# Performance work log

Measured on AMD Instinct MI355X. Metric: run time of the kernel, lower is better.

The kernel has to match this reference:

```python
import jax, jax.numpy as jnp
import numpy as np

LN_EPS = 1e-5


def _ln(x, g, b):
    m = x.mean(-1, keepdims=True)
    v = ((x - m) ** 2).mean(-1, keepdims=True)
    return (x - m) * jax.lax.rsqrt(v + LN_EPS) * g + b


def _shift(x):
    # token shift: previous timestep, zeros at t=0. x: [B,T,C]
    return jnp.pad(x[:, :-1], ((0, 0), (1, 0), (0, 0)))


def _wkv(time_decay, time_first, k, v):
    # numerically-stable RWKV-v4 WKV scan. k, v: [B,T,C]
    B, T, C = k.shape
    decay = -jnp.exp(time_decay)  # [C], negative per-channel log-decay
    kT = jnp.transpose(k, (1, 0, 2))
    vT = jnp.transpose(v, (1, 0, 2))

    def step(carry, kv):
        aa, bb, pp = carry
        kt, vt = kv
        ww = time_first + kt
        p = jnp.maximum(pp, ww)
        e1 = jnp.exp(pp - p)
        e2 = jnp.exp(ww - p)
        out = (e1 * aa + e2 * vt) / (e1 * bb + e2)
        ww2 = pp + decay
        p2 = jnp.maximum(ww2, kt)
        f1 = jnp.exp(ww2 - p2)
        f2 = jnp.exp(kt - p2)
        return (f1 * aa + f2 * vt, f1 * bb + f2, p2), out

    init = (jnp.zeros((B, C), k.dtype), jnp.zeros((B, C), k.dtype),
            jnp.full((B, C), -1e38, k.dtype))
    _, out = jax.lax.scan(step, init, (kT, vT))
    return jnp.transpose(out, (1, 0, 2))


def setup_inputs() -> dict:
    key = jax.random.key(0)
    ks = jax.random.split(key, 24)
    B, T, Dv, Di = 32, 512, 512, 256
    F = Dv + Di
    H = 4 * F
    n = jax.random.normal
    u = jax.random.uniform(ks[4], (B, T, F, 2), minval=1e-6, maxval=1.0 - 1e-6)
    gumbel = -jnp.log(-jnp.log(u))
    sF = 1.0 / np.sqrt(F).astype(np.float32)
    sH = 1.0 / np.sqrt(H).astype(np.float32)
    return {
        'fv': n(ks[0], (B, T, Dv)),
        'fi': n(ks[1], (B, T, Di)),
        'fuse_W': n(ks[2], (F, 2 * F)) * sF,
        'fuse_b': jnp.zeros((2 * F,)),
        'gumbel': gumbel,
        'ln1_g': jnp.ones((F,)), 'ln1_b': jnp.zeros((F,)),
        'mix_k': jax.random.uniform(ks[5], (F,)),
        'mix_v': jax.random.uniform(ks[6], (F,)),
        'mix_r': jax.random.uniform(ks[7], (F,)),
        'time_decay': n(ks[8], (F,)) * 0.1 - 1.0,
        'time_first': n(ks[9], (F,)) * 0.1,
        'Wk': n(ks[10], (F, F)) * sF,
        'Wv': n(ks[11], (F, F)) * sF,
        'Wr': n(ks[12], (F, F)) * sF,
        'Wo': n(ks[13], (F, F)) * sF,
        'ln2_g': jnp.ones((F,)), 'ln2_b': jnp.zeros((F,)),
        'cmix_k': jax.random.uniform(ks[14], (F,)),
        'cmix_r': jax.random.uniform(ks[15], (F,)),
        'cWk': n(ks[16], (F, H)) * sF,
        'cWv': n(ks[17], (H, F)) * sH,
        'cWr': n(ks[18], (F, F)) * sF,
        'reg_W1': n(ks[19], (F, 128)) * sF,
        'reg_b1': jnp.zeros((128,)),
        'reg_W2': n(ks[20], (128, 6)) / np.sqrt(128).astype(np.float32),
        'reg_b2': jnp.zeros((6,)),
    }


def reference(fv, fi, fuse_W, fuse_b, gumbel, ln1_g, ln1_b, mix_k, mix_v, mix_r,
              time_decay, time_first, Wk, Wv, Wr, Wo, ln2_g, ln2_b,
              cmix_k, cmix_r, cWk, cWv, cWr, reg_W1, reg_b1, reg_W2, reg_b2):
    B, T, _ = fv.shape
    # ---- Fusion_module ('hard'): linear -> gumbel-softmax(hard, tau=1) gating
    feat = jnp.concatenate([fv, fi], axis=-1)            # [B,T,F]
    F = feat.shape[-1]
    logits = (feat @ fuse_W + fuse_b).reshape(B, T, F, 2)
    y = jax.nn.softmax(logits + gumbel, axis=-1)          # tau = 1
    hard = jax.nn.one_hot(jnp.argmax(y, -1), 2, dtype=y.dtype)
    mask = hard + y - jax.lax.stop_gradient(y)            # straight-through
    x = feat * mask[..., 0]

    # ---- RWKV block: time-mixing (WKV scan)
    xn = _ln(x, ln1_g, ln1_b)
    xs = _shift(xn)
    xk = xn * mix_k + xs * (1.0 - mix_k)
    xv = xn * mix_v + xs * (1.0 - mix_v)
    xr = xn * mix_r + xs * (1.0 - mix_r)
    k = xk @ Wk
    v = xv @ Wv
    r = jax.nn.sigmoid(xr @ Wr)
    x = x + (r * _wkv(time_decay, time_first, k, v)) @ Wo

    # ---- RWKV block: channel-mixing
    xn = _ln(x, ln2_g, ln2_b)
    xs = _shift(xn)
    xk = xn * cmix_k + xs * (1.0 - cmix_k)
    xr = xn * cmix_r + xs * (1.0 - cmix_r)
    kk = jnp.square(jax.nn.relu(xk @ cWk))
    x = x + jax.nn.sigmoid(xr @ cWr) * (kk @ cWv)

    h = x @ reg_W1 + reg_b1
    h = jnp.where(h > 0, h, 0.1 * h)
    return h @ reg_W2 + reg_b2                            # [B,T,6]
```

## Files before the change

kernel.cpp:

```cpp
#include <hip/hip_runtime.h>
#include <hip/hip_bf16.h>

#define BT 16384
#define FDIM 768
#define HDIM 3072

typedef __attribute__((ext_vector_type(8))) short bf16x8;
typedef __attribute__((ext_vector_type(4))) float f32x4;
typedef __attribute__((ext_vector_type(4))) int i32x4;
typedef __attribute__((ext_vector_type(2))) float f32x2;

__device__ inline float b2f(unsigned short u) {
  union { unsigned int i; float f; } x; x.i = ((unsigned int)u) << 16; return x.f;
}

#define GLOAD16(gptr, lptr)                                                    \
  __builtin_amdgcn_global_load_lds(                                            \
      (const __attribute__((address_space(1))) void*)(gptr),                   \
      (__attribute__((address_space(3))) void*)(lptr), 16, 0, 0)

__global__ void wconv5_kernel(const float* s0, const float* s1, const float* s2,
                              const float* s3, const float* s4,
                              __hip_bfloat16* d0, __hip_bfloat16* d1, __hip_bfloat16* d2,
                              __hip_bfloat16* d3, __hip_bfloat16* d4) {
  const float* in; __hip_bfloat16* out;
  switch (blockIdx.z) {
    case 0: in = s0; out = d0; break;
    case 1: in = s1; out = d1; break;
    case 2: in = s2; out = d2; break;
    case 3: in = s3; out = d3; break;
    default: in = s4; out = d4; break;
  }
  __shared__ float tile[32][33];
  int kb = blockIdx.x * 32, nb = blockIdx.y * 32;
  int tx = threadIdx.x & 31, ty = threadIdx.x >> 5;
#pragma unroll
  for (int i = 0; i < 4; ++i) {
    int k = ty + i * 8;
    tile[k][tx] = in[(size_t)(kb + k) * 768 + nb + tx];
  }
  __syncthreads();
#pragma unroll
  for (int i = 0; i < 4; ++i) {
    int n = ty + i * 8;
    out[(size_t)(nb + n) * 768 + kb + tx] = __float2bfloat16(tile[tx][n]);
  }
}

__global__ void wconv_kernel(const float* __restrict__ in, __hip_bfloat16* __restrict__ out,
                             int K, int N) {
  __shared__ float tile[32][33];
  int kb = blockIdx.x * 32, nb = blockIdx.y * 32;
  int tx = threadIdx.x & 31, ty = threadIdx.x >> 5;
#pragma unroll
  for (int i = 0; i < 4; ++i) {
    int k = ty + i * 8;
    tile[k][tx] = in[(size_t)(kb + k) * N + nb + tx];
  }
  __syncthreads();
#pragma unroll
  for (int i = 0; i < 4; ++i) {
    int n = ty + i * 8;
    out[(size_t)(nb + n) * K + kb + tx] = __float2bfloat16(tile[tx][n]);
  }
}

__global__ void wdsplit_kernel(const float* __restrict__ W, __hip_bfloat16* __restrict__ out) {
  __shared__ float tile[32][33];
  int kb = blockIdx.x * 32, nb = blockIdx.y * 32;
  int tx = threadIdx.x & 31, ty = threadIdx.x >> 5;
#pragma unroll
  for (int i = 0; i < 4; ++i) {
    int k = ty + i * 8;
    f32x2 p = ((const f32x2*)(W + (size_t)(kb + k) * 1536))[nb + tx];
    tile[k][tx] = p.x - p.y;
  }
  __syncthreads();
#pragma unroll
  for (int i = 0; i < 4; ++i) {
    int n = ty + i * 8;
    float d = tile[tx][n];
    __hip_bfloat16 h1 = __float2bfloat16(d);
    float r1 = d - __bfloat162float(h1);
    __hip_bfloat16 h2 = __float2bfloat16(r1);
    float r2 = r1 - __bfloat162float(h2);
    __hip_bfloat16 h3 = __float2bfloat16(r2);
    size_t base = (size_t)(nb + n) * 2304 + kb + tx;
    out[base] = h1; out[base + 768] = h2; out[base + 1536] = h3;
  }
}

__global__ void featsplit_kernel(const float* __restrict__ fv, const float* __restrict__ fi,
                                 __hip_bfloat16* __restrict__ FS) {
  int idx4 = blockIdx.x * 256 + threadIdx.x;
  int m = idx4 / 192, q = idx4 - m * 192;
  int c0 = q * 4;
  f32x4 f;
  if (c0 < 512) f = *(const f32x4*)(fv + (size_t)m * 512 + c0);
  else          f = *(const f32x4*)(fi + (size_t)m * 256 + (c0 - 512));
  unsigned short h1[4], h2[4], h3[4];
#pragma unroll
  for (int j = 0; j < 4; ++j) {
    float x = f[j];
    __hip_bfloat16 a = __float2bfloat16(x);
    float r1 = x - __bfloat162float(a);
    __hip_bfloat16 b = __float2bfloat16(r1);
    float r2 = r1 - __bfloat162float(b);
    __hip_bfloat16 c = __float2bfloat16(r2);
    h1[j] = *(unsigned short*)&a; h2[j] = *(unsigned short*)&b; h3[j] = *(unsigned short*)&c;
  }
  size_t base = (size_t)m * 2304 + c0;
  *(ushort4*)((unsigned short*)FS + base)        = make_ushort4(h1[0], h1[1], h1[2], h1[3]);
  *(ushort4*)((unsigned short*)FS + base + 768)  = make_ushort4(h2[0], h2[1], h2[2], h2[3]);
  *(ushort4*)((unsigned short*)FS + base + 1536) = make_ushort4(h3[0], h3[1], h3[2], h3[3]);
}

__global__ void lnmix3_kernel(const float* __restrict__ X, const float* __restrict__ g,
                              const float* __restrict__ b, const float* __restrict__ mk,
                              const float* __restrict__ mv, const float* __restrict__ mr,
                              __hip_bfloat16* __restrict__ AK, __hip_bfloat16* __restrict__ AV,
                              __hip_bfloat16* __restrict__ AR) {
  __shared__ float xn[5][768];
  int tok0 = blockIdx.x * 4;
  int w = threadIdx.x >> 6, lane = threadIdx.x & 63;
  int t = tok0 + w - 1;
  if (t >= 0) {
    const float* row = X + (size_t)t * 768;
    float vv[12]; float s = 0.f, s2 = 0.f;
#pragma unroll
    for (int i = 0; i < 12; ++i) { float x = row[lane + i * 64]; vv[i] = x; s += x; s2 += x * x; }
#pragma unroll
    for (int o = 32; o; o >>= 1) { s += __shfl_xor(s, o); s2 += __shfl_xor(s2, o); }
    float m = s * (1.0f / 768.0f);
    float var = s2 * (1.0f / 768.0f) - m * m;
    float inv = 1.0f / sqrtf(var + 1e-5f);
#pragma unroll
    for (int i = 0; i < 12; ++i) { int c = lane + i * 64; xn[w][c] = (vv[i] - m) * inv * g[c] + b[c]; }
  }
  __syncthreads();
  if (w >= 1) {
    int tt = tok0 + (w - 1);
    bool first = (tt & 511) == 0;
    size_t base = (size_t)tt * 768;
#pragma unroll
    for (int i = 0; i < 12; ++i) {
      int c = lane + i * 64;
      float a = xn[w][c];
      float sft = first ? 0.0f : xn[w - 1][c];
      float k = mk[c], v = mv[c], r = mr[c];
      AK[base + c] = __float2bfloat16(a * k + sft * (1.0f - k));
      AV[base + c] = __float2bfloat16(a * v + sft * (1.0f - v));
      AR[base + c] = __float2bfloat16(a * r + sft * (1.0f - r));
    }
  }
}

__global__ void lnmix2_kernel(const float* __restrict__ X, const float* __restrict__ g,
                              const float* __restrict__ b, const float* __restrict__ mk,
                              const float* __restrict__ mr,
                              __hip_bfloat16* __restrict__ AK, __hip_bfloat16* __restrict__ AR) {
  __shared__ float xn[5][768];
  int tok0 = blockIdx.x * 4;
  int w = threadIdx.x >> 6, lane = threadIdx.x & 63;
  int t = tok0 + w - 1;
  if (t >= 0) {
    const float* row = X + (size_t)t * 768;
    float vv[12]; float s = 0.f, s2 = 0.f;
#pragma unroll
    for (int i = 0; i < 12; ++i) { float x = row[lane + i * 64]; vv[i] = x; s += x; s2 += x * x; }
#pragma unroll
    for (int o = 32; o; o >>= 1) { s += __shfl_xor(s, o); s2 += __shfl_xor(s2, o); }
    float m = s * (1.0f / 768.0f);
    float var = s2 * (1.0f / 768.0f) - m * m;
    float inv = 1.0f / sqrtf(var + 1e-5f);
#pragma unroll
    for (int i = 0; i < 12; ++i) { int c = lane + i * 64; xn[w][c] = (vv[i] - m) * inv * g[c] + b[c]; }
  }
  __syncthreads();
  if (w >= 1) {
    int tt = tok0 + (w - 1);
    bool first = (tt & 511) == 0;
    size_t base = (size_t)tt * 768;
#pragma unroll
    for (int i = 0; i < 12; ++i) {
      int c = lane + i * 64;
      float a = xn[w][c];
      float sft = first ? 0.0f : xn[w - 1][c];
      float k = mk[c], r = mr[c];
      AK[base + c] = __float2bfloat16(a * k + sft * (1.0f - k));
      AR[base + c] = __float2bfloat16(a * r + sft * (1.0f - r));
    }
  }
}

__global__ void wkv_kernel(const float* __restrict__ K, const float* __restrict__ V,
                           const float* __restrict__ RP, const float* __restrict__ td,
                           const float* __restrict__ tfirst, __hip_bfloat16* __restrict__ RA) {
  int idx = blockIdx.x * 256 + threadIdx.x;
  int b = idx / 768, c = idx - b * 768;
  float decay = -__expf(td[c]);
  float u = tfirst[c];
  float aa = 0.f, bb = 0.f, pp = -1e38f;
  size_t o = (size_t)b * 512 * 768 + c;
  float ck[4], cv[4], cr[4], nk[4], nv[4], nr[4];
#pragma unroll
  for (int j = 0; j < 4; ++j) { size_t oj = o + (size_t)j * 768; ck[j] = K[oj]; cv[j] = V[oj]; cr[j] = RP[oj]; }
  size_t ob = o;
  for (int g = 0; g < 128; ++g) {
    size_t onext = (g == 127) ? o : ob + 3072;
#pragma unroll
    for (int j = 0; j < 4; ++j) {
      size_t oj = onext + (size_t)j * 768;
      nk[j] = K[oj]; nv[j] = V[oj]; nr[j] = RP[oj];
    }
#pragma unroll
    for (int j = 0; j < 4; ++j) {
      float kt = ck[j], vt = cv[j];
      float ww = u + kt;
      float p = fmaxf(pp, ww);
      float e1 = __expf(pp - p), e2 = __expf(ww - p);
      float wkv = (e1 * aa + e2 * vt) / (e1 * bb + e2);
      float ww2 = pp + decay;
      float p2 = fmaxf(ww2, kt);
      float f1 = __expf(ww2 - p2), f2 = __expf(kt - p2);
      aa = f1 * aa + f2 * vt; bb = f1 * bb + f2; pp = p2;
      float r = 1.0f / (1.0f + __expf(-cr[j]));
      RA[ob + (size_t)j * 768] = __float2bfloat16(r * wkv);
    }
#pragma unroll
    for (int j = 0; j < 4; ++j) { ck[j] = nk[j]; cv[j] = nv[j]; cr[j] = nr[j]; }
    ob += 3072;
  }
}

__global__ void reg2_kernel(const __hip_bfloat16* __restrict__ Hb, const float* __restrict__ W2,
                            const float* __restrict__ b2, float* __restrict__ out) {
  __shared__ float w[768];
  for (int i = threadIdx.x; i < 768; i += 256) w[i] = W2[i];
  __syncthreads();
  int m = blockIdx.x * 256 + threadIdx.x;
  float acc[6];
#pragma unroll
  for (int j = 0; j < 6; ++j) acc[j] = b2[j];
  const bf16x8* hr8 = (const bf16x8*)(Hb + (size_t)m * 128);
#pragma unroll
  for (int h8 = 0; h8 < 16; ++h8) {
    bf16x8 pk = hr8[h8];
#pragma unroll
    for (int e = 0; e < 8; ++e) {
      float hv = b2f((unsigned short)pk[e]);
      int h = h8 * 8 + e;
#pragma unroll
      for (int j = 0; j < 6; ++j) acc[j] += hv * w[h * 6 + j];
    }
  }
#pragma unroll
  for (int j = 0; j < 6; ++j) out[(size_t)m * 6 + j] = acc[j];
}

enum { EP_NONE = 0, EP_GATE, EP_RESID, EP_RELUSQ, EP_SIGRESID, EP_LEAKY };

template<int EP, bool SPLIT6>
__global__ void gemm_bt(const __hip_bfloat16* __restrict__ A, const __hip_bfloat16* __restrict__ Bt,
                        int N, int Kphys, int Klog,
                        size_t aZ, size_t bZ, size_t oZ,
                        float* __restrict__ outF, __hip_bfloat16* __restrict__ outH,
                        const float* __restrict__ x0, const float* __restrict__ x1,
                        const float* __restrict__ x2, const float* __restrict__ x3) {
  __shared__ __align__(16) unsigned short sA[128 * 64];
  __shared__ __align__(16) unsigned short sB[128 * 64];
  const int tid = threadIdx.x;
  const int lane = tid & 63;
  const int wid = tid >> 6;
  const int tm = blockIdx.x * 128, tn = blockIdx.y * 128;
  const int wr = (wid >> 1) * 64, wc = (wid & 1) * 64;
  const int r16 = lane & 15, kg = lane >> 4;
  const int z = blockIdx.z;
  A += (size_t)z * aZ; Bt += (size_t)z * bZ;

  f32x4 acc[4][4];
  f32x4 zero = {0.f, 0.f, 0.f, 0.f};
#pragma unroll
  for (int i = 0; i < 4; ++i)
#pragma unroll
    for (int j = 0; j < 4; ++j) acc[i][j] = zero;

  size_t gA[4], gB[4];
  int ldsOff[4];
#pragma unroll
  for (int i = 0; i < 4; ++i) {
    int c = (wid << 2) | i;
    int row = (c << 3) | (lane >> 3);
    int swz = ((lane & 7) ^ (row & 7)) << 3;
    gA[i] = (size_t)(tm + row) * Kphys + swz;
    gB[i] = (size_t)(tn + row) * Kphys + swz;
    ldsOff[i] = c << 9;
  }
  const int ca0 = ((kg ^ (r16 & 7)) << 4);
  const int ca1 = (((4 | kg) ^ (r16 & 7)) << 4);
  const int arow = (wr + r16) * 128;
  const int brow = (wc + r16) * 128;

  const int nsteps = Klog / 64;
  for (int st = 0; st < nsteps; ++st) {
    int k0 = st * 64;
    int kA, kB2;
    if (SPLIT6) {
      static constexpr int mapA[6] = {0, 0, 0, 1, 1, 2};
      static constexpr int mapB[6] = {0, 1, 2, 0, 1, 0};
      int s = k0 / 768; int kr = k0 - s * 768;
      kA = mapA[s] * 768 + kr; kB2 = mapB[s] * 768 + kr;
    } else { kA = k0; kB2 = k0; }
#pragma unroll
    for (int i = 0; i < 4; ++i) GLOAD16(A + gA[i] + kA, sA + ldsOff[i]);
#pragma unroll
    for (int i = 0; i < 4; ++i) GLOAD16(Bt + gB[i] + kB2, sB + ldsOff[i]);
    __syncthreads();
#pragma unroll
    for (int ks = 0; ks < 2; ++ks) {
      const int ca = ks ? ca1 : ca0;
      bf16x8 af[4], bfv[4];
#pragma unroll
      for (int f = 0; f < 4; ++f) {
        af[f]  = *(const bf16x8*)((const char*)sA + arow + f * 2048 + ca);
        bfv[f] = *(const bf16x8*)((const char*)sB + brow + f * 2048 + ca);
      }
#pragma unroll
      for (int fm = 0; fm < 4; ++fm)
#pragma unroll
        for (int fn = 0; fn < 4; ++fn)
          acc[fm][fn] = __builtin_amdgcn_mfma_f32_16x16x32_bf16(af[fm], bfv[fn], acc[fm][fn], 0, 0, 0);
    }
    __syncthreads();
  }

  const int er0 = tm + wr + (lane >> 4) * 4;
  const int ec0 = tn + wc + (lane & 15);
#pragma unroll
  for (int fm = 0; fm < 4; ++fm) {
#pragma unroll
    for (int fn = 0; fn < 4; ++fn) {
#pragma unroll
      for (int j = 0; j < 4; ++j) {
        int row = er0 + fm * 16 + j;
        int col = ec0 + fn * 16;
        float v = acc[fm][fn][j];
        size_t o = (size_t)row * N + col;
        if (EP == EP_NONE) {
          outF[(size_t)z * oZ + o] = v;
        } else if (EP == EP_RESID) {
          outF[o] += v;
        } else if (EP == EP_GATE) {
          size_t gi = ((size_t)row * 768 + col) * 2;
          float gd = x0[gi] - x0[gi + 1];
          float bd = x3[2 * col] - x3[2 * col + 1];
          float s = v + bd + gd;
          float feat = (col < 512) ? x1[(size_t)row * 512 + col]
                                   : x2[(size_t)row * 256 + col - 512];
          outF[o] = (s >= 0.0f) ? feat : 0.0f;
        } else if (EP == EP_RELUSQ) {
          float r = v > 0.f ? v : 0.f;
          outH[o] = __float2bfloat16(r * r);
        } else if (EP == EP_SIGRESID) {
          float sg = 1.0f / (1.0f + __expf(-x0[o]));
          float xv = x1[o] + sg * v;
          outH[o] = __float2bfloat16(xv);
        } else if (EP == EP_LEAKY) {
          float h = v + x0[col];
          h = h > 0.f ? h : 0.1f * h;
          outH[o] = __float2bfloat16(h);
        }
      }
    }
  }
}

extern "C" void kernel_launch(void* const* d_in, const int* in_sizes, int n_in,
                              void* d_out, int out_size, void* d_ws, size_t ws_size,
                              hipStream_t stream) {
  const float* fv     = (const float*)d_in[0];
  const float* fi     = (const float*)d_in[1];
  const float* fuse_W = (const float*)d_in[2];
  const float* fuse_b = (const float*)d_in[3];
  const float* gumbel = (const float*)d_in[4];
  const float* ln1_g  = (const float*)d_in[5];
  const float* ln1_b  = (const float*)d_in[6];
  const float* mix_k  = (const float*)d_in[7];
  const float* mix_v  = (const float*)d_in[8];
  const float* mix_r  = (const float*)d_in[9];
  const float* td     = (const float*)d_in[10];
  const float* tfirst = (const float*)d_in[11];
  const float* Wk     = (const float*)d_in[12];
  const float* Wv     = (const float*)d_in[13];
  const float* Wr     = (const float*)d_in[14];
  const float* Wo     = (const float*)d_in[15];
  const float* ln2_g  = (const float*)d_in[16];
  const float* ln2_b  = (const float*)d_in[17];
  const float* cmk    = (const float*)d_in[18];
  const float* cmr    = (const float*)d_in[19];
  const float* cWk    = (const float*)d_in[20];
  const float* cWv    = (const float*)d_in[21];
  const float* cWr    = (const float*)d_in[22];
  const float* rW1    = (const float*)d_in[23];
  const float* rb1    = (const float*)d_in[24];
  const float* rW2    = (const float*)d_in[25];
  const float* rb2    = (const float*)d_in[26];

  char* ws = (char*)d_ws;
  float* X  = (float*)(ws + 0);
  float* Kb = (float*)(ws + 100663296UL);
  float* RP = (float*)(ws + 201326592UL);
  __hip_bfloat16* AK  = (__hip_bfloat16*)(ws + 251658240UL);
  __hip_bfloat16* AV  = (__hip_bfloat16*)(ws + 276824064UL);
  __hip_bfloat16* AR  = (__hip_bfloat16*)(ws + 301989888UL);
  __hip_bfloat16* RA  = (__hip_bfloat16*)(ws + 327155712UL);
  __hip_bfloat16* Hb  = (__hip_bfloat16*)(ws + 352321536UL);
  __hip_bfloat16* WdT = (__hip_bfloat16*)(ws + 356515840UL);
  __hip_bfloat16* WkT = (__hip_bfloat16*)(ws + 360054784UL);
  __hip_bfloat16* cWkT = (__hip_bfloat16*)(ws + 364773376UL);
  __hip_bfloat16* cWvT = (__hip_bfloat16*)(ws + 369491968UL);
  __hip_bfloat16* cWrT = (__hip_bfloat16*)(ws + 374210560UL);
  __hip_bfloat16* W1T  = (__hip_bfloat16*)(ws + 375390208UL);
  __hip_bfloat16* WvT = (__hip_bfloat16*)(ws + 361234432UL);
  __hip_bfloat16* WrT = (__hip_bfloat16*)(ws + 362414080UL);
  __hip_bfloat16* WoT = (__hip_bfloat16*)(ws + 363593728UL);
  __hip_bfloat16* FS = (__hip_bfloat16*)(ws + 100663296UL);
  __hip_bfloat16* KK = (__hip_bfloat16*)(ws + 100663296UL);

  dim3 blk(256);

  wconv5_kernel<<<dim3(24, 24, 5), blk, 0, stream>>>(Wk, Wv, Wr, Wo, cWr,
                                                     WkT, WvT, WrT, WoT, cWrT);
  wconv_kernel<<<dim3(24, 96), blk, 0, stream>>>(cWk, cWkT, 768, 3072);
  wconv_kernel<<<dim3(96, 24), blk, 0, stream>>>(cWv, cWvT, 3072, 768);
  wconv_kernel<<<dim3(24, 4),  blk, 0, stream>>>(rW1, W1T, 768, 128);
  wdsplit_kernel<<<dim3(24, 24), blk, 0, stream>>>(fuse_W, WdT);

  featsplit_kernel<<<12288, blk, 0, stream>>>(fv, fi, FS);
  gemm_bt<EP_GATE, true><<<dim3(128, 6, 1), blk, 0, stream>>>(
      FS, WdT, 768, 2304, 4608, 0, 0, 0, X, nullptr, gumbel, fv, fi, fuse_b);

  lnmix3_kernel<<<4096, dim3(320), 0, stream>>>(X, ln1_g, ln1_b, mix_k, mix_v, mix_r, AK, AV, AR);
  gemm_bt<EP_NONE, false><<<dim3(128, 6, 3), blk, 0, stream>>>(
      AK, WkT, 768, 768, 768, 12582912UL, 589824UL, 12582912UL,
      Kb, nullptr, nullptr, nullptr, nullptr, nullptr);
  wkv_kernel<<<96, blk, 0, stream>>>(Kb, Kb + 12582912UL, RP, td, tfirst, RA);
  gemm_bt<EP_RESID, false><<<dim3(128, 6, 1), blk, 0, stream>>>(
      RA, WoT, 768, 768, 768, 0, 0, 0, X, nullptr, nullptr, nullptr, nullptr, nullptr);

  lnmix2_kernel<<<4096, dim3(320), 0, stream>>>(X, ln2_g, ln2_b, cmk, cmr, AK, AR);
  gemm_bt<EP_RELUSQ, false><<<dim3(128, 24, 1), blk, 0, stream>>>(
      AK, cWkT, 3072, 768, 768, 0, 0, 0, nullptr, KK, nullptr, nullptr, nullptr, nullptr);
  gemm_bt<EP_NONE, false><<<dim3(128, 6, 1), blk, 0, stream>>>(
      AR, cWrT, 768, 768, 768, 0, 0, 0, RP, nullptr, nullptr, nullptr, nullptr, nullptr);
  gemm_bt<EP_SIGRESID, false><<<dim3(128, 6, 1), blk, 0, stream>>>(
      KK, cWvT, 768, 3072, 3072, 0, 0, 0, nullptr, AV, RP, X, nullptr, nullptr);

  gemm_bt<EP_LEAKY, false><<<dim3(128, 1, 1), blk, 0, stream>>>(
      AV, W1T, 128, 768, 768, 0, 0, 0, nullptr, Hb, rb1, nullptr, nullptr, nullptr);
  reg2_kernel<<<64, blk, 0, stream>>>(Hb, rW2, rb2, (float*)d_out);
}
```

Baseline: 934.0 us.

## Double-buffer GEMM LDS tiles and remap workgroups across XCDs

Changes the bf16 GEMM main loop to double-buffered LDS stages, so global-to-LDS loads for the next K step are issued before the MFMA compute on the current buffer. This hides load latency and removes one barrier per step. The launch grid is flattened to 1D, and block IDs are remapped so that consecutive workgroups on the same XCD (w&7 grouping) cover neighbouring tiles, which should improve L2 reuse. LDS use doubles to 64KB per block, which may lower occupancy, and the loop assumes an even number of K steps.

```diff
diff --git a/kernel.cpp b/kernel.cpp
--- a/kernel.cpp
+++ b/kernel.cpp
@@ -262,17 +262,25 @@
 
 template<int EP, bool SPLIT6>
 __global__ void gemm_bt(const __hip_bfloat16* __restrict__ A, const __hip_bfloat16* __restrict__ Bt,
-                        int N, int Kphys, int Klog,
+                        int N, int Kphys, int Klog, int ny,
                         size_t aZ, size_t bZ, size_t oZ,
                         float* __restrict__ outF, __hip_bfloat16* __restrict__ outH,
                         const float* __restrict__ x0, const float* __restrict__ x1,
                         const float* __restrict__ x2, const float* __restrict__ x3) {
-  __shared__ __align__(16) unsigned short sA[128 * 64];
-  __shared__ __align__(16) unsigned short sB[128 * 64];
+  __shared__ __align__(16) unsigned short sA0[8192];
+  __shared__ __align__(16) unsigned short sB0[8192];
+  __shared__ __align__(16) unsigned short sA1[8192];
+  __shared__ __align__(16) unsigned short sB1[8192];
   const int tid = threadIdx.x;
   const int lane = tid & 63;
   const int wid = tid >> 6;
-  const int tm = blockIdx.x * 128, tn = blockIdx.y * 128;
+
+  const int w = blockIdx.x;
+  const int nwg = gridDim.x;
+  const int wp = (w & 7) * (nwg >> 3) + (w >> 3);
+  const int bx = wp / ny, by = wp - bx * ny;
+  const int tm = bx * 128, tn = by * 128;
+
   const int wr = (wid >> 1) * 64, wc = (wid & 1) * 64;
   const int r16 = lane & 15, kg = lane >> 4;
   const int z = blockIdx.z;
@@ -301,8 +309,7 @@
   const int arow = (wr + r16) * 128;
   const int brow = (wc + r16) * 128;
 
-  const int nsteps = Klog / 64;
-  for (int st = 0; st < nsteps; ++st) {
+  auto STAGE = [&](unsigned short* dA, unsigned short* dB, int st) {
     int k0 = st * 64;
     int kA, kB2;
     if (SPLIT6) {
@@ -312,18 +319,20 @@
       kA = mapA[s] * 768 + kr; kB2 = mapB[s] * 768 + kr;
     } else { kA = k0; kB2 = k0; }
 #pragma unroll
-    for (int i = 0; i < 4; ++i) GLOAD16(A + gA[i] + kA, sA + ldsOff[i]);
-#pragma unroll
-    for (int i = 0; i < 4; ++i) GLOAD16(Bt + gB[i] + kB2, sB + ldsOff[i]);
-    __syncthreads();
+    for (int i = 0; i < 4; ++i) GLOAD16(A + gA[i] + kA, dA + ldsOff[i]);
+#pragma unroll
+    for (int i = 0; i < 4; ++i) GLOAD16(Bt + gB[i] + kB2, dB + ldsOff[i]);
+  };
+
+  auto COMPUTE = [&](const unsigned short* cA, const unsigned short* cB) {
 #pragma unroll
     for (int ks = 0; ks < 2; ++ks) {
       const int ca = ks ? ca1 : ca0;
       bf16x8 af[4], bfv[4];
 #pragma unroll
       for (int f = 0; f < 4; ++f) {
-        af[f]  = *(const bf16x8*)((const char*)sA + arow + f * 2048 + ca);
-        bfv[f] = *(const bf16x8*)((const char*)sB + brow + f * 2048 + ca);
+        af[f]  = *(const bf16x8*)((const char*)cA + arow + f * 2048 + ca);
+        bfv[f] = *(const bf16x8*)((const char*)cB + brow + f * 2048 + ca);
       }
 #pragma unroll
       for (int fm = 0; fm < 4; ++fm)
@@ -331,6 +340,17 @@
         for (int fn = 0; fn < 4; ++fn)
           acc[fm][fn] = __builtin_amdgcn_mfma_f32_16x16x32_bf16(af[fm], bfv[fn], acc[fm][fn], 0, 0, 0);
     }
+  };
+
+  const int nsteps = Klog / 64;
+  STAGE(sA0, sB0, 0);
+  __syncthreads();
+  for (int st = 0; st + 2 <= nsteps; st += 2) {
+    STAGE(sA1, sB1, st + 1);
+    COMPUTE(sA0, sB0);
+    __syncthreads();
+    if (st + 2 < nsteps) STAGE(sA0, sB0, st + 2);
+    COMPUTE(sA1, sB1);
     __syncthreads();
   }
 
@@ -437,26 +457,26 @@
   wdsplit_kernel<<<dim3(24, 24), blk, 0, stream>>>(fuse_W, WdT);
 
   featsplit_kernel<<<12288, blk, 0, stream>>>(fv, fi, FS);
-  gemm_bt<EP_GATE, true><<<dim3(128, 6, 1), blk, 0, stream>>>(
-      FS, WdT, 768, 2304, 4608, 0, 0, 0, X, nullptr, gumbel, fv, fi, fuse_b);
+  gemm_bt<EP_GATE, true><<<dim3(768, 1, 1), blk, 0, stream>>>(
+      FS, WdT, 768, 2304, 4608, 6, 0, 0, 0, X, nullptr, gumbel, fv, fi, fuse_b);
 
   lnmix3_kernel<<<4096, dim3(320), 0, stream>>>(X, ln1_g, ln1_b, mix_k, mix_v, mix_r, AK, AV, AR);
-  gemm_bt<EP_NONE, false><<<dim3(128, 6, 3), blk, 0, stream>>>(
-      AK, WkT, 768, 768, 768, 12582912UL, 589824UL, 12582912UL,
+  gemm_bt<EP_NONE, false><<<dim3(768, 1, 3), blk, 0, stream>>>(
+      AK, WkT, 768, 768, 768, 6, 12582912UL, 589824UL, 12582912UL,
       Kb, nullptr, nullptr, nullptr, nullptr, nullptr);
   wkv_kernel<<<96, blk, 0, stream>>>(Kb, Kb + 12582912UL, RP, td, tfirst, RA);
-  gemm_bt<EP_RESID, false><<<dim3(128, 6, 1), blk, 0, stream>>>(
-      RA, WoT, 768, 768, 768, 0, 0, 0, X, nullptr, nullptr, nullptr, nullptr, nullptr);
+  gemm_bt<EP_RESID, false><<<dim3(768, 1, 1), blk, 0, stream>>>(
+      RA, WoT, 768, 768, 768, 6, 0, 0, 0, X, nullptr, nullptr, nullptr, nullptr, nullptr);
 
   lnmix2_kernel<<<4096, dim3(320), 0, stream>>>(X, ln2_g, ln2_b, cmk, cmr, AK, AR);
-  gemm_bt<EP_RELUSQ, false><<<dim3(128, 24, 1), blk, 0, stream>>>(
-      AK, cWkT, 3072, 768, 768, 0, 0, 0, nullptr, KK, nullptr, nullptr, nullptr, nullptr);
-  gemm_bt<EP_NONE, false><<<dim3(128, 6, 1), blk, 0, stream>>>(
-      AR, cWrT, 768, 768, 768, 0, 0, 0, RP, nullptr, nullptr, nullptr, nullptr, nullptr);
-  gemm_bt<EP_SIGRESID, false><<<dim3(128, 6, 1), blk, 0, stream>>>(
-      KK, cWvT, 768, 3072, 3072, 0, 0, 0, nullptr, AV, RP, X, nullptr, nullptr);
+  gemm_bt<EP_RELUSQ, false><<<dim3(3072, 1, 1), blk, 0, stream>>>(
+      AK, cWkT, 3072, 768, 768, 24, 0, 0, 0, nullptr, KK, nullptr, nullptr, nullptr, nullptr);
+  gemm_bt<EP_NONE, false><<<dim3(768, 1, 1), blk, 0, stream>>>(
+      AR, cWrT, 768, 768, 768, 6, 0, 0, 0, RP, nullptr, nullptr, nullptr, nullptr, nullptr);
+  gemm_bt<EP_SIGRESID, false><<<dim3(768, 1, 1), blk, 0, stream>>>(
+      KK, cWvT, 768, 3072, 3072, 6, 0, 0, 0, nullptr, AV, RP, X, nullptr, nullptr);
 
   gemm_bt<EP_LEAKY, false><<<dim3(128, 1, 1), blk, 0, stream>>>(
-      AV, W1T, 128, 768, 768, 0, 0, 0, nullptr, Hb, rb1, nullptr, nullptr, nullptr);
+      AV, W1T, 128, 768, 768, 1, 0, 0, 0, nullptr, Hb, rb1, nullptr, nullptr, nullptr);
   reg2_kernel<<<64, blk, 0, stream>>>(Hb, rW2, rb2, (float*)d_out);
 }
```

After: 1.757 ms. 1.88x slower.
